# Kernel tuning notes

Measured on AMD Instinct MI355X. Metric: run time of the kernel, lower is better.

## Reference

```python
import jax, jax.numpy as jnp
import numpy as np

N_NODES = 50000
N_EDGES = 800000
N_GRAPHS = 64


def setup_inputs() -> dict:
    key = jax.random.key(0)
    ks = jax.random.split(key, 16)
    x = jax.random.normal(ks[0], (N_NODES, 3), dtype=jnp.float32)
    edge_index = jax.random.randint(ks[1], (2, N_EDGES), 0, N_NODES, dtype=jnp.int32)
    batch = jnp.sort(jax.random.randint(ks[2], (N_NODES,), 0, N_GRAPHS, dtype=jnp.int32))
    def glorot(k, shape):
        fan_in, fan_out = shape
        lim = (6.0 / (fan_in + fan_out)) ** 0.5
        return jax.random.uniform(k, shape, jnp.float32, -lim, lim)
    return {
        "x": x,
        "edge_index": edge_index,
        "batch": batch,
        "W1": glorot(ks[3], (3, 64)),   "b1": jnp.zeros((64,), jnp.float32),
        "W2": glorot(ks[4], (64, 128)), "b2": jnp.zeros((128,), jnp.float32),
        "W3": glorot(ks[5], (128, 128)),"b3": jnp.zeros((128,), jnp.float32),
        "Wf1": glorot(ks[6], (128, 64)),"bf1": jnp.zeros((64,), jnp.float32),
        "Wf2": glorot(ks[7], (64, 10)), "bf2": jnp.zeros((10,), jnp.float32),
    }


def _gcn_conv(h, src, dst, norm, W, b, n_nodes):
    h = h @ W                                   # [N, out]
    msg = h[src] * norm[:, None]                # gather + scale  [E+N, out]
    agg = jax.ops.segment_sum(msg, dst, num_segments=n_nodes)  # scatter-add
    return agg + b


def reference(x, edge_index, batch, W1, b1, W2, b2, W3, b3, Wf1, bf1, Wf2, bf2):
    n = x.shape[0]
    loop = jnp.arange(n, dtype=edge_index.dtype)
    src = jnp.concatenate([edge_index[0], loop])  # add self-loops once
    dst = jnp.concatenate([edge_index[1], loop])
    deg = jax.ops.segment_sum(jnp.ones_like(dst, jnp.float32), dst, num_segments=n)
    dinv = jax.lax.rsqrt(deg)                     # deg >= 1 (self-loops)
    norm = dinv[src] * dinv[dst]

    h = jax.nn.relu(_gcn_conv(x, src, dst, norm, W1, b1, n))
    h = jax.nn.relu(_gcn_conv(h, src, dst, norm, W2, b2, n))
    h = jax.nn.relu(_gcn_conv(h, src, dst, norm, W3, b3, n))

    # global mean pool over graphs in the batch
    sums = jax.ops.segment_sum(h, batch, num_segments=N_GRAPHS)      # [G, 128]
    cnts = jax.ops.segment_sum(jnp.ones((n,), jnp.float32), batch, num_segments=N_GRAPHS)
    pooled = sums / jnp.maximum(cnts, 1.0)[:, None]

    h = jax.nn.relu(pooled @ Wf1 + bf1)
    return h @ Wf2 + bf2  # dropout is identity at inference
```

## Files before the change

### kernel.cpp

```cpp
#include <hip/hip_runtime.h>

#define N_NODES 50000
#define N_EDGES 800000
#define N_GRAPHS 64
#define SCAN_B 256
#define SCAN_NBLK ((N_NODES + SCAN_B - 1) / SCAN_B)
#define FILL_E 2048

typedef __attribute__((ext_vector_type(8))) short short8;
typedef __attribute__((ext_vector_type(4))) float floatx4;

__device__ __forceinline__ unsigned short f2bf(float f) {
    unsigned int u = __float_as_uint(f);
    u += 0x7FFFu + ((u >> 16) & 1u);
    return (unsigned short)(u >> 16);
}
__device__ __forceinline__ float bf2f(unsigned short h) {
    return __uint_as_float(((unsigned int)h) << 16);
}
__device__ __forceinline__ float blo(unsigned int u) { return __uint_as_float(u << 16); }
__device__ __forceinline__ float bhi(unsigned int u) { return __uint_as_float(u & 0xffff0000u); }


__global__ void k_prep(int* counts, float* pooled,
                       const float* __restrict__ W2, const float* __restrict__ W3,
                       unsigned short* Wb2, unsigned short* Wb3) {
    int i = blockIdx.x * blockDim.x + threadIdx.x;
    if (i < N_NODES) counts[i] = 0;
    int j = i - N_NODES;
    if (j >= 0 && j < N_GRAPHS * 128) pooled[j] = 0.0f;
    int k = i - N_NODES - N_GRAPHS * 128;
    if (k >= 0 && k < 64 * 128) {
        int kk = k >> 7, n = k & 127;
        Wb2[(((kk >> 3) * 128) + n) * 8 + (kk & 7)] = f2bf(W2[k]);
    }
    int l = i - N_NODES - N_GRAPHS * 128 - 64 * 128;
    if (l >= 0 && l < 128 * 128) {
        int kk = l >> 7, n = l & 127;
        Wb3[(((kk >> 3) * 128) + n) * 8 + (kk & 7)] = f2bf(W3[l]);
    }
}


__global__ void k_hist(const int* __restrict__ dst, int* counts) {
    int i = blockIdx.x * blockDim.x + threadIdx.x;
    if (i < N_EDGES) atomicAdd(&counts[dst[i]], 1);
}

__global__ void k_scan1(const int* __restrict__ counts, int* row_ptr, int* blksum) {
    __shared__ int s[SCAN_B];
    int i = blockIdx.x * SCAN_B + threadIdx.x;
    int c = (i < N_NODES) ? counts[i] : 0;
    s[threadIdx.x] = c;
    __syncthreads();
    for (int off = 1; off < SCAN_B; off <<= 1) {
        int v = (threadIdx.x >= off) ? s[threadIdx.x - off] : 0;
        __syncthreads();
        s[threadIdx.x] += v;
        __syncthreads();
    }
    if (i < N_NODES) row_ptr[i] = s[threadIdx.x] - c;
    if (threadIdx.x == SCAN_B - 1) blksum[blockIdx.x] = s[SCAN_B - 1];
}

__global__ void k_scan3(int* row_ptr, const int* __restrict__ blksum,
                        int* bcursor, const int* __restrict__ counts, float* dinv,
                        const float* __restrict__ x, float* __restrict__ xs) {
    __shared__ int s[SCAN_B];
    int t = threadIdx.x;
    int b = blockIdx.x;
    s[t] = (t < b && t < SCAN_NBLK) ? blksum[t] : 0;
    __syncthreads();
    for (int off = SCAN_B / 2; off > 0; off >>= 1) {
        if (t < off) s[t] += s[t + off];
        __syncthreads();
    }
    int offset = s[0];
    if (t == 0) bcursor[b] = offset;
    int i = b * SCAN_B + t;
    if (i < N_NODES) {
        row_ptr[i] += offset;
        float di = rsqrtf((float)(counts[i] + 1));
        dinv[i] = di;
        xs[i * 3 + 0] = x[i * 3 + 0] * di;
        xs[i * 3 + 1] = x[i * 3 + 1] * di;
        xs[i * 3 + 2] = x[i * 3 + 2] * di;
    }
    if (i == 0) row_ptr[N_NODES] = N_EDGES;
}

__global__ __launch_bounds__(256) void k_binfill(const int* __restrict__ src,
                                                 const int* __restrict__ dst,
                                                 int* bcursor, int2* __restrict__ bpair) {
    __shared__ int cnt[SCAN_B];
    __shared__ int sc[SCAN_B];
    __shared__ int base[SCAN_B];
    __shared__ int delta[SCAN_B];
    __shared__ int ofs[SCAN_B];
    __shared__ int2 stage[FILL_E];
    __shared__ unsigned char bk[FILL_E];
    int tid = threadIdx.x;
    int e0 = blockIdx.x * FILL_E + tid * 8;
    cnt[tid] = 0; ofs[tid] = 0;
    __syncthreads();
    int s[8], d[8], bb[8];
    bool active = e0 < N_EDGES;
    if (active) {
        int4 sa = *(const int4*)(src + e0);
        int4 sb = *(const int4*)(src + e0 + 4);
        int4 da = *(const int4*)(dst + e0);
        int4 db = *(const int4*)(dst + e0 + 4);
        s[0]=sa.x; s[1]=sa.y; s[2]=sa.z; s[3]=sa.w;
        s[4]=sb.x; s[5]=sb.y; s[6]=sb.z; s[7]=sb.w;
        d[0]=da.x; d[1]=da.y; d[2]=da.z; d[3]=da.w;
        d[4]=db.x; d[5]=db.y; d[6]=db.z; d[7]=db.w;
#pragma unroll
        for (int k = 0; k < 8; ++k) {
            bb[k] = d[k] >> 8;
            atomicAdd(&cnt[bb[k]], 1);
        }
    }
    __syncthreads();
    int c = cnt[tid];
    sc[tid] = c;
    __syncthreads();
    for (int off = 1; off < SCAN_B; off <<= 1) {
        int v = (tid >= off) ? sc[tid - off] : 0;
        __syncthreads();
        sc[tid] += v;
        __syncthreads();
    }
    base[tid] = sc[tid] - c;
    if (c > 0) delta[tid] = atomicAdd(&bcursor[tid], c) - base[tid];
    __syncthreads();
    if (active) {
#pragma unroll
        for (int k = 0; k < 8; ++k) {
            int p = base[bb[k]] + atomicAdd(&ofs[bb[k]], 1);
            stage[p] = make_int2(s[k], d[k]);
            bk[p] = (unsigned char)bb[k];
        }
    }
    __syncthreads();
    int total = base[SCAN_B - 1] + cnt[SCAN_B - 1];
    for (int i = tid; i < total; i += 256)
        bpair[delta[bk[i]] + i] = stage[i];
}

__global__ __launch_bounds__(256) void k_fill2(const int2* __restrict__ bpair,
                                               const int* __restrict__ row_ptr,
                                               int* __restrict__ csr_src) {
    __shared__ int cur[SCAN_B];
    int b = blockIdx.x;
    int t = threadIdx.x;
    int n0 = b * SCAN_B;
    int n = n0 + t;
    cur[t] = (n < N_NODES) ? row_ptr[n] : 0;
    int start = row_ptr[n0];
    int endn = (n0 + SCAN_B < N_NODES) ? (n0 + SCAN_B) : N_NODES;
    int end = row_ptr[endn];
    __syncthreads();
    for (int i = start + t; i < end; i += 256) {
        int2 pr = bpair[i];
        int pos = atomicAdd(&cur[pr.y & (SCAN_B - 1)], 1);
        csr_src[pos] = pr.x;
    }
}


__global__ void k_agg3(const float* __restrict__ xs, const int* __restrict__ row_ptr,
                       const int* __restrict__ csr_src, const float* __restrict__ dinv,
                       float* __restrict__ out) {
    int n = blockIdx.x * blockDim.x + threadIdx.x;
    if (n >= N_NODES) return;
    int lo = row_ptr[n], hi = row_ptr[n + 1];
    float a0 = xs[n * 3 + 0], a1 = xs[n * 3 + 1], a2 = xs[n * 3 + 2];
    for (int i = lo; i < hi; ++i) {
        int s = csr_src[i];
        a0 += xs[s * 3 + 0];
        a1 += xs[s * 3 + 1];
        a2 += xs[s * 3 + 2];
    }
    float din = dinv[n];
    out[n * 3 + 0] = a0 * din;
    out[n * 3 + 1] = a1 * din;
    out[n * 3 + 2] = a2 * din;
}

template<int IN_W, int OUT_W, int NPB>
__global__ void k_node_gemm(const float* __restrict__ h, const float* __restrict__ W,
                            const float* __restrict__ b, const float* __restrict__ dinv,
                            unsigned short* __restrict__ hb) {
    __shared__ float rows[NPB][IN_W];
    int n0 = blockIdx.x * NPB;
    int j = threadIdx.x;
    for (int t = j; t < NPB * IN_W; t += OUT_W) {
        int m = t / IN_W, k = t - m * IN_W;
        int n = n0 + m;
        rows[m][k] = (n < N_NODES) ? h[(size_t)n * IN_W + k] : 0.0f;
    }
    __syncthreads();
    float acc[NPB];
    float bj = b[j];
#pragma unroll
    for (int m = 0; m < NPB; ++m) acc[m] = bj;
#pragma unroll
    for (int k = 0; k < IN_W; ++k) {
        float wk = W[k * OUT_W + j];
#pragma unroll
        for (int m = 0; m < NPB; ++m) acc[m] += rows[m][k] * wk;
    }
#pragma unroll
    for (int m = 0; m < NPB; ++m) {
        int n = n0 + m;
        if (n < N_NODES)
            hb[(size_t)n * OUT_W + j] = f2bf(fmaxf(acc[m], 0.0f) * dinv[n]);
    }
}


__global__ void k_agg64(const unsigned short* __restrict__ hb, const int* __restrict__ row_ptr,
                        const int* __restrict__ csr_src, const float* __restrict__ dinv,
                        unsigned short* __restrict__ outb) {
    int wv = (blockIdx.x * blockDim.x + threadIdx.x) >> 6;
    int lane = threadIdx.x & 63;
    if (wv >= N_NODES) return;
    int q = lane & 7;
    int slot = lane >> 3;
    int lo = row_ptr[wv], hi = row_ptr[wv + 1];
    const uint4* hbv = (const uint4*)hb;
    float acc[8];
#pragma unroll
    for (int i = 0; i < 8; ++i) acc[i] = 0.f;
    if (slot == 0) {
        uint4 u = hbv[(size_t)wv * 8 + q];
        acc[0] += blo(u.x); acc[1] += bhi(u.x);
        acc[2] += blo(u.y); acc[3] += bhi(u.y);
        acc[4] += blo(u.z); acc[5] += bhi(u.z);
        acc[6] += blo(u.w); acc[7] += bhi(u.w);
    }
    for (int base = lo; base < hi; base += 32) {
#pragma unroll
        for (int k = 0; k < 4; ++k) {
            int e = base + k * 8 + slot;
            int ee = e < hi ? e : hi - 1;
            int s = csr_src[ee];
            uint4 u = hbv[(size_t)s * 8 + q];
            if (e < hi) {
                acc[0] += blo(u.x); acc[1] += bhi(u.x);
                acc[2] += blo(u.y); acc[3] += bhi(u.y);
                acc[4] += blo(u.z); acc[5] += bhi(u.z);
                acc[6] += blo(u.w); acc[7] += bhi(u.w);
            }
        }
    }
#pragma unroll
    for (int i = 0; i < 8; ++i) {
        acc[i] += __shfl_xor(acc[i], 8);
        acc[i] += __shfl_xor(acc[i], 16);
        acc[i] += __shfl_xor(acc[i], 32);
    }
    if (slot == 0) {
        float din = dinv[wv];
        uint4 w;
        w.x = (unsigned int)f2bf(acc[0] * din) | ((unsigned int)f2bf(acc[1] * din) << 16);
        w.y = (unsigned int)f2bf(acc[2] * din) | ((unsigned int)f2bf(acc[3] * din) << 16);
        w.z = (unsigned int)f2bf(acc[4] * din) | ((unsigned int)f2bf(acc[5] * din) << 16);
        w.w = (unsigned int)f2bf(acc[6] * din) | ((unsigned int)f2bf(acc[7] * din) << 16);
        ((uint4*)outb)[(size_t)wv * 8 + q] = w;
    }
}

__global__ void k_agg128(const unsigned short* __restrict__ hb, const int* __restrict__ row_ptr,
                         const int* __restrict__ csr_src, const float* __restrict__ dinv,
                         unsigned short* __restrict__ outb) {
    int wv = (blockIdx.x * blockDim.x + threadIdx.x) >> 6;
    int lane = threadIdx.x & 63;
    if (wv >= N_NODES) return;
    int q = lane & 15;
    int slot = lane >> 4;
    int lo = row_ptr[wv], hi = row_ptr[wv + 1];
    const uint4* hbv = (const uint4*)hb;
    float acc[8];
#pragma unroll
    for (int i = 0; i < 8; ++i) acc[i] = 0.f;
    if (slot == 0) {
        uint4 u = hbv[(size_t)wv * 16 + q];
        acc[0] += blo(u.x); acc[1] += bhi(u.x);
        acc[2] += blo(u.y); acc[3] += bhi(u.y);
        acc[4] += blo(u.z); acc[5] += bhi(u.z);
        acc[6] += blo(u.w); acc[7] += bhi(u.w);
    }
    for (int base = lo; base < hi; base += 16) {
#pragma unroll
        for (int k = 0; k < 4; ++k) {
            int e = base + k * 4 + slot;
            int ee = e < hi ? e : hi - 1;
            int s = csr_src[ee];
            uint4 u = hbv[(size_t)s * 16 + q];
            if (e < hi) {
                acc[0] += blo(u.x); acc[1] += bhi(u.x);
                acc[2] += blo(u.y); acc[3] += bhi(u.y);
                acc[4] += blo(u.z); acc[5] += bhi(u.z);
                acc[6] += blo(u.w); acc[7] += bhi(u.w);
            }
        }
    }
#pragma unroll
    for (int i = 0; i < 8; ++i) {
        acc[i] += __shfl_xor(acc[i], 16);
        acc[i] += __shfl_xor(acc[i], 32);
    }
    if (slot == 0) {
        float din = dinv[wv];
        uint4 w;
        w.x = (unsigned int)f2bf(acc[0] * din) | ((unsigned int)f2bf(acc[1] * din) << 16);
        w.y = (unsigned int)f2bf(acc[2] * din) | ((unsigned int)f2bf(acc[3] * din) << 16);
        w.z = (unsigned int)f2bf(acc[4] * din) | ((unsigned int)f2bf(acc[5] * din) << 16);
        w.w = (unsigned int)f2bf(acc[6] * din) | ((unsigned int)f2bf(acc[7] * din) << 16);
        ((uint4*)outb)[(size_t)wv * 16 + q] = w;
    }
}


__global__ __launch_bounds__(256) void k_gemm_l2_mfma(
    const unsigned short* __restrict__ Ab,
    const unsigned short* __restrict__ Wb,
    const float* __restrict__ b,
    const float* __restrict__ dinv,
    unsigned short* __restrict__ hb) {
    __shared__ float sC[64][128];
    int tid = threadIdx.x;
    int wave = tid >> 6, lane = tid & 63;
    int quad = lane >> 4, l16 = lane & 15;
    int n0 = blockIdx.x * 64;
    int arow = n0 + wave * 16 + l16;
    if (arow >= N_NODES) arow = N_NODES - 1;

    floatx4 acc[8];
#pragma unroll
    for (int t = 0; t < 8; ++t) acc[t] = (floatx4){0.f, 0.f, 0.f, 0.f};

#pragma unroll
    for (int ks = 0; ks < 2; ++ks) {
        short8 a = *(const short8*)(Ab + (size_t)arow * 64 + ks * 32 + quad * 8);
#pragma unroll
        for (int t = 0; t < 8; ++t) {
            short8 bf = *(const short8*)(Wb + (((ks * 4 + quad) * 128) + t * 16 + l16) * 8);
            acc[t] = __builtin_amdgcn_mfma_f32_16x16x32_bf16(a, bf, acc[t], 0, 0, 0);
        }
    }
#pragma unroll
    for (int t = 0; t < 8; ++t)
#pragma unroll
        for (int r = 0; r < 4; ++r)
            sC[wave * 16 + quad * 4 + r][t * 16 + l16] = acc[t][r];
    __syncthreads();
    int tn = tid >> 5, tj = tid & 31;
    float4 bv = *(const float4*)(b + tj * 4);
#pragma unroll
    for (int m = 0; m < 8; ++m) {
        int n = n0 + tn * 8 + m;
        if (n < N_NODES) {
            float di = dinv[n];
            unsigned short h0 = f2bf(fmaxf(sC[tn * 8 + m][tj * 4 + 0] + bv.x, 0.f) * di);
            unsigned short h1 = f2bf(fmaxf(sC[tn * 8 + m][tj * 4 + 1] + bv.y, 0.f) * di);
            unsigned short h2 = f2bf(fmaxf(sC[tn * 8 + m][tj * 4 + 2] + bv.z, 0.f) * di);
            unsigned short h3 = f2bf(fmaxf(sC[tn * 8 + m][tj * 4 + 3] + bv.w, 0.f) * di);
            uint2 w2;
            w2.x = (unsigned int)h0 | ((unsigned int)h1 << 16);
            w2.y = (unsigned int)h2 | ((unsigned int)h3 << 16);
            *(uint2*)(hb + (size_t)n * 128 + tj * 4) = w2;
        }
    }
}


__global__ __launch_bounds__(256) void k_gemm_l3_mfma_pool(
    const unsigned short* __restrict__ Ab,
    const unsigned short* __restrict__ Wb,
    const float* __restrict__ b,
    const int* __restrict__ batch,
    float* __restrict__ pooled) {
    __shared__ float sC[64][128];
    __shared__ float red[8][128];
    __shared__ int sb[64];
    int tid = threadIdx.x;
    int wave = tid >> 6, lane = tid & 63;
    int quad = lane >> 4, l16 = lane & 15;
    int n0 = blockIdx.x * 64;
    int arow = n0 + wave * 16 + l16;
    if (arow >= N_NODES) arow = N_NODES - 1;

    floatx4 acc[8];
#pragma unroll
    for (int t = 0; t < 8; ++t) acc[t] = (floatx4){0.f, 0.f, 0.f, 0.f};

#pragma unroll
    for (int ks = 0; ks < 4; ++ks) {
        short8 a = *(const short8*)(Ab + (size_t)arow * 128 + ks * 32 + quad * 8);
#pragma unroll
        for (int t = 0; t < 8; ++t) {
            short8 bf = *(const short8*)(Wb + (((ks * 4 + quad) * 128) + t * 16 + l16) * 8);
            acc[t] = __builtin_amdgcn_mfma_f32_16x16x32_bf16(a, bf, acc[t], 0, 0, 0);
        }
    }
#pragma unroll
    for (int t = 0; t < 8; ++t) {
        float bc = b[t * 16 + l16];
#pragma unroll
        for (int r = 0; r < 4; ++r)
            sC[wave * 16 + quad * 4 + r][t * 16 + l16] = fmaxf(acc[t][r] + bc, 0.f);
    }
    if (tid < 64) {
        int n = n0 + tid;
        sb[tid] = (n < N_NODES) ? batch[n] : -1;
    }
    __syncthreads();
    int g0 = sb[0];
    int last = (n0 + 63 < N_NODES) ? (n0 + 63) : (N_NODES - 1);
    int g1 = batch[last];
    int tn = tid >> 5, tj = tid & 31;
    for (int g = g0; g <= g1; ++g) {
        float p0 = 0.f, p1 = 0.f, p2 = 0.f, p3 = 0.f;
#pragma unroll
        for (int m = 0; m < 8; ++m) {
            if (sb[tn * 8 + m] == g) {
                p0 += sC[tn * 8 + m][tj * 4 + 0];
                p1 += sC[tn * 8 + m][tj * 4 + 1];
                p2 += sC[tn * 8 + m][tj * 4 + 2];
                p3 += sC[tn * 8 + m][tj * 4 + 3];
            }
        }
        red[tn][tj * 4 + 0] = p0;
        red[tn][tj * 4 + 1] = p1;
        red[tn][tj * 4 + 2] = p2;
        red[tn][tj * 4 + 3] = p3;
        __syncthreads();
        if (tid < 128) {
            float s = 0.f;
#pragma unroll
            for (int r = 0; r < 8; ++r) s += red[r][tid];
            atomicAdd(&pooled[g * 128 + tid], s);
        }
        __syncthreads();
    }
}


__device__ __forceinline__ int lower_bound_batch(const int* __restrict__ batch, int val) {
    int lo = 0, hi = N_NODES;
    while (lo < hi) {
        int mid = (lo + hi) >> 1;
        if (batch[mid] < val) lo = mid + 1; else hi = mid;
    }
    return lo;
}

__global__ void k_fc(const float* __restrict__ pooled, const int* __restrict__ batch,
                     const float* __restrict__ Wf1, const float* __restrict__ bf1,
                     const float* __restrict__ Wf2, const float* __restrict__ bf2,
                     float* __restrict__ out) {
    __shared__ float sp[128];
    __shared__ float sh1[64];
    int g = blockIdx.x;
    int t = threadIdx.x;
    int lo = lower_bound_batch(batch, g);
    int hi = lower_bound_batch(batch, g + 1);
    float inv = 1.0f / fmaxf((float)(hi - lo), 1.0f);
    sp[t] = pooled[g * 128 + t] * inv;
    __syncthreads();
    if (t < 64) {
        float acc = bf1[t];
#pragma unroll 8
        for (int k = 0; k < 128; ++k) acc += sp[k] * Wf1[k * 64 + t];
        sh1[t] = fmaxf(acc, 0.0f);
    }
    __syncthreads();
    if (t < 10) {
        float acc = bf2[t];
#pragma unroll 8
        for (int k = 0; k < 64; ++k) acc += sh1[k] * Wf2[k * 10 + t];
        out[g * 10 + t] = acc;
    }
}

extern "C" void kernel_launch(void* const* d_in, const int* in_sizes, int n_in,
                              void* d_out, int out_size, void* d_ws, size_t ws_size,
                              hipStream_t stream) {
    const float* x     = (const float*)d_in[0];
    const int*   ei    = (const int*)d_in[1];
    const int*   batch = (const int*)d_in[2];
    const float* W1  = (const float*)d_in[3];
    const float* b1  = (const float*)d_in[4];
    const float* W2  = (const float*)d_in[5];
    const float* b2  = (const float*)d_in[6];
    const float* W3  = (const float*)d_in[7];
    const float* b3  = (const float*)d_in[8];
    const float* Wf1 = (const float*)d_in[9];
    const float* bf1 = (const float*)d_in[10];
    const float* Wf2 = (const float*)d_in[11];
    const float* bf2 = (const float*)d_in[12];
    float* out = (float*)d_out;

    const int* src = ei;
    const int* dst = ei + N_EDGES;

    float* dinv   = (float*)d_ws;
    int*   counts = (int*)(dinv + N_NODES);
    int*   row_ptr= counts + N_NODES;
    int*   blksum = row_ptr + N_NODES + 1;
    int*   bcursor= blksum + 256;
    int*   csr_src= bcursor + 256;
    int2*  bpair  = (int2*)(csr_src + N_EDGES);
    float* xs     = (float*)(bpair + N_EDGES);
    float* a3     = xs + (size_t)N_NODES * 3;
    unsigned short* Wb2 = (unsigned short*)(a3 + (size_t)N_NODES * 3);
    unsigned short* Wb3 = Wb2 + 64 * 128;
    size_t ofs = (size_t)(Wb3 + 128 * 128) - (size_t)d_ws;
    ofs = (ofs + 15) & ~(size_t)15;
    unsigned short* bufA = (unsigned short*)((char*)d_ws + ofs);
    unsigned short* hb   = bufA + (size_t)N_NODES * 128;
    float* pooled = (float*)(hb + (size_t)N_NODES * 128);

    const int TB = 256;
    const int GEMM_BLKS = (N_NODES + 63) / 64;
    const int PREP_N = N_NODES + N_GRAPHS * 128 + 64 * 128 + 128 * 128;
    const int BIN_BLKS = (N_EDGES + FILL_E - 1) / FILL_E;

    k_prep<<<(PREP_N + TB - 1) / TB, TB, 0, stream>>>(counts, pooled, W2, W3, Wb2, Wb3);
    k_hist<<<(N_EDGES + TB - 1) / TB, TB, 0, stream>>>(dst, counts);
    k_scan1<<<SCAN_NBLK, SCAN_B, 0, stream>>>(counts, row_ptr, blksum);
    k_scan3<<<SCAN_NBLK, SCAN_B, 0, stream>>>(row_ptr, blksum, bcursor, counts, dinv, x, xs);
    k_binfill<<<BIN_BLKS, 256, 0, stream>>>(src, dst, bcursor, bpair);
    k_fill2<<<SCAN_NBLK, 256, 0, stream>>>(bpair, row_ptr, csr_src);

    k_agg3<<<(N_NODES + TB - 1) / TB, TB, 0, stream>>>(xs, row_ptr, csr_src, dinv, a3);
    k_node_gemm<3, 64, 4><<<(N_NODES + 3) / 4, 64, 0, stream>>>(a3, W1, b1, dinv, hb);

    k_agg64<<<(N_NODES * 64 + TB - 1) / TB, TB, 0, stream>>>(hb, row_ptr, csr_src, dinv, bufA);
    k_gemm_l2_mfma<<<GEMM_BLKS, 256, 0, stream>>>(bufA, Wb2, b2, dinv, hb);

    k_agg128<<<(N_NODES * 64 + TB - 1) / TB, TB, 0, stream>>>(hb, row_ptr, csr_src, dinv, bufA);
    k_gemm_l3_mfma_pool<<<GEMM_BLKS, 256, 0, stream>>>(bufA, Wb3, b3, batch, pooled);

    k_fc<<<N_GRAPHS, 128, 0, stream>>>(pooled, batch, Wf1, bf1, Wf2, bf2, out);
}
```

Measured before the change: 268.9 us.

## Replace per-node histogram and scans with coarse bucket histogram and in-block CSR build

Replaces the per-node global atomic histogram and two-pass scan with a shared-memory histogram over 256-node buckets, a single-block bucket scan, and a build kernel that counts per-node degrees within each bucket, scans them locally, and writes row_ptr, dinv and scaled features alongside the CSR fill. This removes 800K global atomics and one launch, and drops the 50K-entry counts clear. In exchange, the build kernel reads its bucket of bpair twice.

```diff
diff --git a/kernel.cpp b/kernel.cpp
--- a/kernel.cpp
+++ b/kernel.cpp
@@ -22,19 +22,19 @@
 __device__ __forceinline__ float bhi(unsigned int u) { return __uint_as_float(u & 0xffff0000u); }
 
 
-__global__ void k_prep(int* counts, float* pooled,
+__global__ void k_prep(int* bcnt, float* pooled,
                        const float* __restrict__ W2, const float* __restrict__ W3,
                        unsigned short* Wb2, unsigned short* Wb3) {
     int i = blockIdx.x * blockDim.x + threadIdx.x;
-    if (i < N_NODES) counts[i] = 0;
-    int j = i - N_NODES;
+    if (i < 256) bcnt[i] = 0;
+    int j = i - 256;
     if (j >= 0 && j < N_GRAPHS * 128) pooled[j] = 0.0f;
-    int k = i - N_NODES - N_GRAPHS * 128;
+    int k = i - 256 - N_GRAPHS * 128;
     if (k >= 0 && k < 64 * 128) {
         int kk = k >> 7, n = k & 127;
         Wb2[(((kk >> 3) * 128) + n) * 8 + (kk & 7)] = f2bf(W2[k]);
     }
-    int l = i - N_NODES - N_GRAPHS * 128 - 64 * 128;
+    int l = i - 256 - N_GRAPHS * 128 - 64 * 128;
     if (l >= 0 && l < 128 * 128) {
         int kk = l >> 7, n = l & 127;
         Wb3[(((kk >> 3) * 128) + n) * 8 + (kk & 7)] = f2bf(W3[l]);
@@ -42,51 +42,41 @@
 }
 
 
-__global__ void k_hist(const int* __restrict__ dst, int* counts) {
-    int i = blockIdx.x * blockDim.x + threadIdx.x;
-    if (i < N_EDGES) atomicAdd(&counts[dst[i]], 1);
-}
-
-__global__ void k_scan1(const int* __restrict__ counts, int* row_ptr, int* blksum) {
-    __shared__ int s[SCAN_B];
-    int i = blockIdx.x * SCAN_B + threadIdx.x;
-    int c = (i < N_NODES) ? counts[i] : 0;
-    s[threadIdx.x] = c;
-    __syncthreads();
-    for (int off = 1; off < SCAN_B; off <<= 1) {
-        int v = (threadIdx.x >= off) ? s[threadIdx.x - off] : 0;
-        __syncthreads();
-        s[threadIdx.x] += v;
-        __syncthreads();
-    }
-    if (i < N_NODES) row_ptr[i] = s[threadIdx.x] - c;
-    if (threadIdx.x == SCAN_B - 1) blksum[blockIdx.x] = s[SCAN_B - 1];
-}
-
-__global__ void k_scan3(int* row_ptr, const int* __restrict__ blksum,
-                        int* bcursor, const int* __restrict__ counts, float* dinv,
-                        const float* __restrict__ x, float* __restrict__ xs) {
-    __shared__ int s[SCAN_B];
+__global__ __launch_bounds__(256) void k_bhist(const int* __restrict__ dst, int* bcnt) {
+    __shared__ int bins[SCAN_NBLK];
     int t = threadIdx.x;
-    int b = blockIdx.x;
-    s[t] = (t < b && t < SCAN_NBLK) ? blksum[t] : 0;
-    __syncthreads();
-    for (int off = SCAN_B / 2; off > 0; off >>= 1) {
-        if (t < off) s[t] += s[t + off];
-        __syncthreads();
-    }
-    int offset = s[0];
-    if (t == 0) bcursor[b] = offset;
-    int i = b * SCAN_B + t;
-    if (i < N_NODES) {
-        row_ptr[i] += offset;
-        float di = rsqrtf((float)(counts[i] + 1));
-        dinv[i] = di;
-        xs[i * 3 + 0] = x[i * 3 + 0] * di;
-        xs[i * 3 + 1] = x[i * 3 + 1] * di;
-        xs[i * 3 + 2] = x[i * 3 + 2] * di;
-    }
-    if (i == 0) row_ptr[N_NODES] = N_EDGES;
+    for (int i = t; i < SCAN_NBLK; i += 256) bins[i] = 0;
+    __syncthreads();
+    int stride = gridDim.x * blockDim.x;
+    for (int i4 = blockIdx.x * blockDim.x + t; i4 < N_EDGES / 4; i4 += stride) {
+        int4 d = ((const int4*)dst)[i4];
+        atomicAdd(&bins[d.x >> 8], 1);
+        atomicAdd(&bins[d.y >> 8], 1);
+        atomicAdd(&bins[d.z >> 8], 1);
+        atomicAdd(&bins[d.w >> 8], 1);
+    }
+    __syncthreads();
+    for (int i = t; i < SCAN_NBLK; i += 256)
+        if (bins[i]) atomicAdd(&bcnt[i], bins[i]);
+}
+
+__global__ __launch_bounds__(256) void k_bscan(const int* __restrict__ bcnt,
+                                               int* bstart, int* bcursor) {
+    __shared__ int s[256];
+    int t = threadIdx.x;
+    int c = (t < SCAN_NBLK) ? bcnt[t] : 0;
+    s[t] = c;
+    __syncthreads();
+    for (int off = 1; off < 256; off <<= 1) {
+        int v = (t >= off) ? s[t - off] : 0;
+        __syncthreads();
+        s[t] += v;
+        __syncthreads();
+    }
+    int excl = s[t] - c;
+    bstart[t] = excl;
+    bcursor[t] = excl;
+    if (t == 255) bstart[256] = s[255];
 }
 
 __global__ __launch_bounds__(256) void k_binfill(const int* __restrict__ src,
@@ -147,23 +137,48 @@
         bpair[delta[bk[i]] + i] = stage[i];
 }
 
-__global__ __launch_bounds__(256) void k_fill2(const int2* __restrict__ bpair,
-                                               const int* __restrict__ row_ptr,
-                                               int* __restrict__ csr_src) {
+__global__ __launch_bounds__(256) void k_build(const int2* __restrict__ bpair,
+                                               const int* __restrict__ bstart,
+                                               int* row_ptr, int* __restrict__ csr_src,
+                                               float* dinv,
+                                               const float* __restrict__ x,
+                                               float* __restrict__ xs) {
+    __shared__ int cnt[SCAN_B];
+    __shared__ int sc[SCAN_B];
     __shared__ int cur[SCAN_B];
-    int b = blockIdx.x;
-    int t = threadIdx.x;
-    int n0 = b * SCAN_B;
-    int n = n0 + t;
-    cur[t] = (n < N_NODES) ? row_ptr[n] : 0;
-    int start = row_ptr[n0];
-    int endn = (n0 + SCAN_B < N_NODES) ? (n0 + SCAN_B) : N_NODES;
-    int end = row_ptr[endn];
+    int b = blockIdx.x, t = threadIdx.x;
+    int start = bstart[b], end = bstart[b + 1];
+    cnt[t] = 0;
+    __syncthreads();
+    for (int i = start + t; i < end; i += 256)
+        atomicAdd(&cnt[bpair[i].y & (SCAN_B - 1)], 1);
+    __syncthreads();
+    int c = cnt[t];
+    sc[t] = c;
+    __syncthreads();
+    for (int off = 1; off < SCAN_B; off <<= 1) {
+        int v = (t >= off) ? sc[t - off] : 0;
+        __syncthreads();
+        sc[t] += v;
+        __syncthreads();
+    }
+    int pos = start + sc[t] - c;
+    cur[t] = pos;
+    int n = b * SCAN_B + t;
+    if (n < N_NODES) {
+        row_ptr[n] = pos;
+        float di = rsqrtf((float)(c + 1));
+        dinv[n] = di;
+        xs[n * 3 + 0] = x[n * 3 + 0] * di;
+        xs[n * 3 + 1] = x[n * 3 + 1] * di;
+        xs[n * 3 + 2] = x[n * 3 + 2] * di;
+    }
+    if (n == N_NODES) row_ptr[N_NODES] = N_EDGES;
     __syncthreads();
     for (int i = start + t; i < end; i += 256) {
         int2 pr = bpair[i];
-        int pos = atomicAdd(&cur[pr.y & (SCAN_B - 1)], 1);
-        csr_src[pos] = pr.x;
+        int p = atomicAdd(&cur[pr.y & (SCAN_B - 1)], 1);
+        csr_src[p] = pr.x;
     }
 }
 
@@ -507,12 +522,14 @@
     const int* dst = ei + N_EDGES;
 
     float* dinv   = (float*)d_ws;
-    int*   counts = (int*)(dinv + N_NODES);
-    int*   row_ptr= counts + N_NODES;
-    int*   blksum = row_ptr + N_NODES + 1;
-    int*   bcursor= blksum + 256;
-    int*   csr_src= bcursor + 256;
-    int2*  bpair  = (int2*)(csr_src + N_EDGES);
+    int*   bcnt   = (int*)(dinv + N_NODES);
+    int*   bstart = bcnt + 256;
+    int*   bcursor= bstart + 257;
+    int*   row_ptr= bcursor + 256;
+    int*   csr_src= row_ptr + N_NODES + 1;
+    size_t o1 = (size_t)(csr_src + N_EDGES) - (size_t)d_ws;
+    o1 = (o1 + 7) & ~(size_t)7;
+    int2*  bpair  = (int2*)((char*)d_ws + o1);
     float* xs     = (float*)(bpair + N_EDGES);
     float* a3     = xs + (size_t)N_NODES * 3;
     unsigned short* Wb2 = (unsigned short*)(a3 + (size_t)N_NODES * 3);
@@ -525,15 +542,14 @@
 
     const int TB = 256;
     const int GEMM_BLKS = (N_NODES + 63) / 64;
-    const int PREP_N = N_NODES + N_GRAPHS * 128 + 64 * 128 + 128 * 128;
+    const int PREP_N = 256 + N_GRAPHS * 128 + 64 * 128 + 128 * 128;
     const int BIN_BLKS = (N_EDGES + FILL_E - 1) / FILL_E;
 
-    k_prep<<<(PREP_N + TB - 1) / TB, TB, 0, stream>>>(counts, pooled, W2, W3, Wb2, Wb3);
-    k_hist<<<(N_EDGES + TB - 1) / TB, TB, 0, stream>>>(dst, counts);
-    k_scan1<<<SCAN_NBLK, SCAN_B, 0, stream>>>(counts, row_ptr, blksum);
-    k_scan3<<<SCAN_NBLK, SCAN_B, 0, stream>>>(row_ptr, blksum, bcursor, counts, dinv, x, xs);
+    k_prep<<<(PREP_N + TB - 1) / TB, TB, 0, stream>>>(bcnt, pooled, W2, W3, Wb2, Wb3);
+    k_bhist<<<256, 256, 0, stream>>>(dst, bcnt);
+    k_bscan<<<1, 256, 0, stream>>>(bcnt, bstart, bcursor);
     k_binfill<<<BIN_BLKS, 256, 0, stream>>>(src, dst, bcursor, bpair);
-    k_fill2<<<SCAN_NBLK, 256, 0, stream>>>(bpair, row_ptr, csr_src);
+    k_build<<<SCAN_NBLK, 256, 0, stream>>>(bpair, bstart, row_ptr, csr_src, dinv, x, xs);
 
     k_agg3<<<(N_NODES + TB - 1) / TB, TB, 0, stream>>>(xs, row_ptr, csr_src, dinv, a3);
     k_node_gemm<3, 64, 4><<<(N_NODES + 3) / 4, 64, 0, stream>>>(a3, W1, b1, dinv, hb);
```

Result: faster. 238.5 us (-11.3%).
